# Optimization experiments

Hardware: AMD Instinct MI355X
Metric: run time of the kernel (lower is better)

## Reference

```python
import jax, jax.numpy as jnp
import numpy as np

B, CIN, H, W = 2, 192, 56, 56
ODIM, HEADS, K, PAD, STRIDE = 192, 6, 7, 3, 1


def setup_inputs() -> dict:
    key = jax.random.key(0)
    ks = jax.random.split(key, 6)
    w_scale = 0.02
    return {
        "x": jax.random.normal(ks[0], (B, CIN, H, W), dtype=jnp.float32),
        "wq": jax.random.normal(ks[1], (ODIM, CIN), dtype=jnp.float32) * w_scale,
        "wk": jax.random.normal(ks[2], (ODIM, CIN), dtype=jnp.float32) * w_scale,
        "wv": jax.random.normal(ks[3], (ODIM, CIN), dtype=jnp.float32) * w_scale,
        "pos_embedding": jax.random.normal(ks[4], (1, 2 * K - 1), dtype=jnp.float32),
        "w_proj": jax.random.normal(ks[5], (ODIM, ODIM), dtype=jnp.float32) * w_scale,
        "kernel_size": K,
        "padding": PAD,
        "stride": STRIDE,
        "num_heads": HEADS,
    }


def _patches(x, k, pad, stride):
    # torch.nn.Unfold(kernel_size=k, padding=pad, stride=stride), kept as
    # (B, C, k*k, oh, ow) with window offsets ordered row-major (i*k + j),
    # channel slowest -- matching torch's (C, kh, kw) flattening.
    xp = jnp.pad(x, ((0, 0), (0, 0), (pad, pad), (pad, pad)))
    Hp, Wp = xp.shape[2], xp.shape[3]
    oh = (Hp - k) // stride + 1
    ow = (Wp - k) // stride + 1
    sl = [xp[:, :, i:i + stride * (oh - 1) + 1:stride, j:j + stride * (ow - 1) + 1:stride]
          for i in range(k) for j in range(k)]
    return jnp.stack(sl, axis=2)


def reference(x, wq, wk, wv, pos_embedding, w_proj, kernel_size, padding, stride, num_heads):
    b, c, h, w = x.shape
    # 1x1 convs (no bias) == channel matmuls
    q = jnp.einsum('oc,bchw->bohw', wq, x)
    k = jnp.einsum('oc,bchw->bohw', wk, x)
    v = jnp.einsum('oc,bchw->bohw', wv, x)
    # Unfold(kernel=1, stride=s) on q == strided spatial subsampling
    q = q[:, :, ::stride, ::stride]
    kp = _patches(k, kernel_size, padding, stride)  # (B, O, K*K, oh, ow)
    vp = _patches(v, kernel_size, padding, stride)
    oh, ow = kp.shape[3], kp.shape[4]
    d = wq.shape[0] // num_heads
    kk = kernel_size * kernel_size
    qh = q.reshape(b, num_heads, d, oh, ow)
    kh = kp.reshape(b, num_heads, d, kk, oh, ow)
    vh = vp.reshape(b, num_heads, d, kk, oh, ow)
    # per-pixel windowed attention scores: (B, heads, K*K, oh, ow)
    attn = jnp.einsum('bhdij,bhdkij->bhkij', qh, kh)
    # relative position bias: index = row_offset + col_offset (0 .. 2K-2)
    coords = np.arange(kernel_size)
    rel = (coords[:, None] + coords[None, :]).reshape(-1)  # (K*K,)
    bias = pos_embedding[0][jnp.asarray(rel)]  # (K*K,)
    attn = jax.nn.softmax(attn + bias[None, None, :, None, None], axis=2)
    out = jnp.einsum('bhkij,bhdkij->bhdij', attn, vh)
    out = out.reshape(b, num_heads * d, oh, ow)
    return jnp.einsum('oc,bchw->bohw', w_proj, out)
```

## Files before the change

### kernel.cpp

```cpp
#include <hip/hip_runtime.h>


#define HW    3136
#define WIMG  56
#define CIN   192
#define QKVLD 576

using short8 = __attribute__((ext_vector_type(8))) short;
using f32x4  = __attribute__((ext_vector_type(4))) float;

__device__ __forceinline__ unsigned short f2bf(float f) {
    union { float f; unsigned int u; } v; v.f = f;
    unsigned int r = v.u + 0x7fffu + ((v.u >> 16) & 1u);
    return (unsigned short)(r >> 16);
}

__global__ __launch_bounds__(256) void prep_kernel(
    const float* __restrict__ x,  const float* __restrict__ wq,
    const float* __restrict__ wk, const float* __restrict__ wv,
    const float* __restrict__ wproj,
    unsigned short* __restrict__ xt, unsigned short* __restrict__ wb)
{
    const int tid = threadIdx.x;
    if (blockIdx.z == 2) {
        int gid  = blockIdx.y * 49 + blockIdx.x;
        int base = (gid * 256 + tid) * 4;
        if (base < 147456) {
            const float* src;
            if      (base <  36864) src = wq    + base;
            else if (base <  73728) src = wk    + base -  36864;
            else if (base < 110592) src = wv    + base -  73728;
            else                    src = wproj + base - 110592;
            float4 v = *(const float4*)src;
            ushort4 h;
            h.x = f2bf(v.x); h.y = f2bf(v.y); h.z = f2bf(v.z); h.w = f2bf(v.w);
            *(ushort4*)(wb + base) = h;
        }
        return;
    }
    __shared__ float t[64][68];
    const int b  = blockIdx.z;
    const int p0 = blockIdx.x * 64, c0 = blockIdx.y * 64;
    {
        const int r0 = tid >> 4, pq = (tid & 15) * 4;
        #pragma unroll
        for (int i = 0; i < 4; ++i) {
            int cc = r0 + 16 * i;
            float4 v = *(const float4*)(x + (size_t)(b * CIN + c0 + cc) * HW + p0 + pq);
            *(float4*)&t[cc][pq] = v;
        }
    }
    __syncthreads();
    #pragma unroll
    for (int i = 0; i < 2; ++i) {
        int u = tid + 256 * i;
        int pr = u >> 3, oct = u & 7;
        ushort4 h0, h1;
        h0.x = f2bf(t[oct*8+0][pr]); h0.y = f2bf(t[oct*8+1][pr]);
        h0.z = f2bf(t[oct*8+2][pr]); h0.w = f2bf(t[oct*8+3][pr]);
        h1.x = f2bf(t[oct*8+4][pr]); h1.y = f2bf(t[oct*8+5][pr]);
        h1.z = f2bf(t[oct*8+6][pr]); h1.w = f2bf(t[oct*8+7][pr]);
        unsigned short* dst = xt + ((size_t)(b * HW + p0 + pr) * CIN + c0 + oct * 8);
        *(ushort4*)dst       = h0;
        *(ushort4*)(dst + 4) = h1;
    }
}

__global__ __launch_bounds__(256) void gemm64(
    const unsigned short* __restrict__ A, long Ab,
    const unsigned short* __restrict__ B, long Bb,
    float* __restrict__ Y, long Yb, int ldY)
{
    __shared__ unsigned short As[64 * 200];
    __shared__ unsigned short Bs[64 * 200];
    const int tid = threadIdx.x;

    A += blockIdx.z * Ab + (size_t)blockIdx.x * 64 * CIN;
    B += blockIdx.z * Bb + (size_t)blockIdx.y * 64 * CIN;
    Y += blockIdx.z * Yb + (size_t)blockIdx.x * 64 * ldY + blockIdx.y * 64;

    const int r = tid >> 2, c4 = tid & 3;
    #pragma unroll
    for (int i = 0; i < 6; ++i) {
        int oct = c4 + 4 * i;
        *(uint4*)(As + r * 200 + oct * 8) = *(const uint4*)(A + r * CIN + oct * 8);
        *(uint4*)(Bs + r * 200 + oct * 8) = *(const uint4*)(B + r * CIN + oct * 8);
    }
    __syncthreads();

    const int lane = tid & 63, wave = tid >> 6;
    const int wm = (wave & 1) * 32, wn = (wave >> 1) * 32;
    const int l15 = lane & 15, quad = lane >> 4;

    f32x4 acc[2][2] = {};
    const unsigned short* pa0 = As + (wm + l15) * 200 + quad * 8;
    const unsigned short* pb0 = Bs + (wn + l15) * 200 + quad * 8;

    #pragma unroll
    for (int s = 0; s < 6; ++s) {
        short8 a0 = *(const short8*)(pa0 + s * 32);
        short8 a1 = *(const short8*)(pa0 + 16 * 200 + s * 32);
        short8 b0 = *(const short8*)(pb0 + s * 32);
        short8 b1 = *(const short8*)(pb0 + 16 * 200 + s * 32);
        acc[0][0] = __builtin_amdgcn_mfma_f32_16x16x32_bf16(a0, b0, acc[0][0], 0, 0, 0);
        acc[0][1] = __builtin_amdgcn_mfma_f32_16x16x32_bf16(a0, b1, acc[0][1], 0, 0, 0);
        acc[1][0] = __builtin_amdgcn_mfma_f32_16x16x32_bf16(a1, b0, acc[1][0], 0, 0, 0);
        acc[1][1] = __builtin_amdgcn_mfma_f32_16x16x32_bf16(a1, b1, acc[1][1], 0, 0, 0);
    }

    #pragma unroll
    for (int ti = 0; ti < 2; ++ti)
        #pragma unroll
        for (int tj = 0; tj < 2; ++tj)
            #pragma unroll
            for (int rr = 0; rr < 4; ++rr) {
                int row = wm + ti * 16 + quad * 4 + rr;
                int col = wn + tj * 16 + l15;
                Y[(size_t)row * ldY + col] = acc[ti][tj][rr];
            }
}

__global__ __launch_bounds__(256) void attn_kernel(
    const float* __restrict__ qkv, const float* __restrict__ pos,
    unsigned short* __restrict__ oact)
{
    __shared__ float kbuf[196 * 34];
    __shared__ float vbuf[196 * 34];

    const int tid = threadIdx.x;
    const int tx = blockIdx.x, ty = blockIdx.y;
    const int b = blockIdx.z / 6, h = blockIdx.z % 6;
    const int y0 = ty * 8 - 3, x0 = tx * 8 - 3;
    const int chk = 192 + h * 32, chv = 384 + h * 32;

    for (int ii = tid; ii < 3136; ii += 256) {
        int pp = ii >> 4, u = ii & 15;
        int py = pp / 14, px = pp - py * 14;
        int gy = y0 + py, gx = x0 + px;
        int isv = u >> 3, uu = u & 7;
        float4 val = make_float4(0.f, 0.f, 0.f, 0.f);
        if ((unsigned)gy < 56u && (unsigned)gx < 56u) {
            int p = gy * WIMG + gx;
            val = *(const float4*)(qkv + (size_t)(b * HW + p) * QKVLD + (isv ? chv : chk) + uu * 4);
        }
        float* dst = (isv ? vbuf : kbuf) + pp * 34 + uu * 4;
        *(float2*)dst       = make_float2(val.x, val.y);
        *(float2*)(dst + 2) = make_float2(val.z, val.w);
    }
    __syncthreads();

    const int sub = tid & 3, pix = tid >> 2;
    const int py = pix >> 3, px = pix & 7;
    const int y = ty * 8 + py, x = tx * 8 + px;
    const int p = y * WIMG + x;

    const float* qb = qkv + (size_t)(b * HW + p) * QKVLD + h * 32 + sub * 8;
    float4 q0 = *(const float4*)qb, q1 = *(const float4*)(qb + 4);

    float posr[13];
    #pragma unroll
    for (int i = 0; i < 13; ++i) posr[i] = pos[i];

    float logits[49];
    #pragma unroll
    for (int kk = 0; kk < 49; ++kk) {
        const int ky = kk / 7, kx = kk % 7;
        const int pp = (py + ky) * 14 + (px + kx);
        const float2* kp = (const float2*)(kbuf + pp * 34 + sub * 8);
        float2 k0 = kp[0], k1 = kp[1], k2 = kp[2], k3 = kp[3];
        float s = 0.f;
        s = fmaf(q0.x, k0.x, s); s = fmaf(q0.y, k0.y, s);
        s = fmaf(q0.z, k1.x, s); s = fmaf(q0.w, k1.y, s);
        s = fmaf(q1.x, k2.x, s); s = fmaf(q1.y, k2.y, s);
        s = fmaf(q1.z, k3.x, s); s = fmaf(q1.w, k3.y, s);
        s += __shfl_xor(s, 1);
        s += __shfl_xor(s, 2);
        logits[kk] = s + posr[ky + kx];
    }

    float m = logits[0];
    #pragma unroll
    for (int kk = 1; kk < 49; ++kk) m = fmaxf(m, logits[kk]);
    float sum = 0.f;
    #pragma unroll
    for (int kk = 0; kk < 49; ++kk) {
        logits[kk] = __expf(logits[kk] - m);
        sum += logits[kk];
    }
    const float inv = 1.f / sum;

    float acc[8] = {};
    #pragma unroll
    for (int kk = 0; kk < 49; ++kk) {
        const int ky = kk / 7, kx = kk % 7;
        const int pp = (py + ky) * 14 + (px + kx);
        const float2* vp = (const float2*)(vbuf + pp * 34 + sub * 8);
        float2 v0 = vp[0], v1 = vp[1], v2 = vp[2], v3 = vp[3];
        const float pw = logits[kk] * inv;
        acc[0] = fmaf(pw, v0.x, acc[0]); acc[1] = fmaf(pw, v0.y, acc[1]);
        acc[2] = fmaf(pw, v1.x, acc[2]); acc[3] = fmaf(pw, v1.y, acc[3]);
        acc[4] = fmaf(pw, v2.x, acc[4]); acc[5] = fmaf(pw, v2.y, acc[5]);
        acc[6] = fmaf(pw, v3.x, acc[6]); acc[7] = fmaf(pw, v3.y, acc[7]);
    }

    ushort4 h0, h1;
    h0.x = f2bf(acc[0]); h0.y = f2bf(acc[1]); h0.z = f2bf(acc[2]); h0.w = f2bf(acc[3]);
    h1.x = f2bf(acc[4]); h1.y = f2bf(acc[5]); h1.z = f2bf(acc[6]); h1.w = f2bf(acc[7]);
    unsigned short* ob = oact + ((size_t)(b * HW + p) * CIN + h * 32 + sub * 8);
    *(ushort4*)ob       = h0;
    *(ushort4*)(ob + 4) = h1;
}

extern "C" void kernel_launch(void* const* d_in, const int* in_sizes, int n_in,
                              void* d_out, int out_size, void* d_ws, size_t ws_size,
                              hipStream_t stream)
{
    const float* x     = (const float*)d_in[0];
    const float* wq    = (const float*)d_in[1];
    const float* wk    = (const float*)d_in[2];
    const float* wv    = (const float*)d_in[3];
    const float* pos   = (const float*)d_in[4];
    const float* wproj = (const float*)d_in[5];

    char* ws = (char*)d_ws;
    unsigned short* xt   = (unsigned short*)(ws);
    unsigned short* wb   = (unsigned short*)(ws + 2408448);
    float*          qkv  = (float*)        (ws + 2703360);
    unsigned short* oact = (unsigned short*)(ws + 17154048);
    float* out = (float*)d_out;

    prep_kernel<<<dim3(49, 3, 3), 256, 0, stream>>>(x, wq, wk, wv, wproj, xt, wb);
    gemm64<<<dim3(49, 9, 2), 256, 0, stream>>>(
        xt, (long)HW * CIN, wb, 0L, qkv, (long)HW * QKVLD, QKVLD);
    attn_kernel<<<dim3(7, 7, 12), 256, 0, stream>>>(qkv, pos, oact);
    gemm64<<<dim3(3, 49, 2), 256, 0, stream>>>(
        wb + 576 * CIN, 0L, oact, (long)HW * CIN, out, (long)CIN * HW, HW);
}
```

Before: 113.4 us.

## Fuse pipeline into one cooperative persistent kernel with grid syncs and bf16 QK

Replaces the four launches (prep, QKV GEMM, attention, projection GEMM) with one cooperative persistent kernel of 256 blocks that loops over tiles in three phases separated by grid.sync. The fp32-to-bf16 conversion of x and the weights now happens inside the GEMM tile loads, so the separate prep pass and its workspace traffic go away. Q and K are stored as bf16 while V stays fp32, which halves the Q/K intermediate traffic at some cost in precision. The aim is to cut launch overhead and memory round trips, at the price of grid-wide barriers and only 256 resident blocks doing all the work. A plain multi-kernel fallback runs if the cooperative launch fails.

```diff
diff --git a/kernel.cpp b/kernel.cpp
--- a/kernel.cpp
+++ b/kernel.cpp
@@ -1,101 +1,82 @@
 #include <hip/hip_runtime.h>
+#include <hip/hip_cooperative_groups.h>
+
+namespace cg = cooperative_groups;
 
 
 #define HW    3136
 #define WIMG  56
 #define CIN   192
-#define QKVLD 576
+#define QKLD  384
+#define SMEM_BYTES 53312
 
 using short8 = __attribute__((ext_vector_type(8))) short;
 using f32x4  = __attribute__((ext_vector_type(4))) float;
 
 __device__ __forceinline__ unsigned short f2bf(float f) {
-    union { float f; unsigned int u; } v; v.f = f;
-    unsigned int r = v.u + 0x7fffu + ((v.u >> 16) & 1u);
+    union { float f; unsigned u; } v; v.f = f;
+    unsigned r = v.u + 0x7fffu + ((v.u >> 16) & 1u);
     return (unsigned short)(r >> 16);
 }
-
-__global__ __launch_bounds__(256) void prep_kernel(
-    const float* __restrict__ x,  const float* __restrict__ wq,
+__device__ __forceinline__ unsigned pack2(float a, float b) {
+    return (unsigned)f2bf(a) | ((unsigned)f2bf(b) << 16);
+}
+__device__ __forceinline__ float bflo(unsigned u) {
+    union { unsigned u; float f; } v; v.u = u << 16; return v.f;
+}
+__device__ __forceinline__ float bfhi(unsigned u) {
+    union { unsigned u; float f; } v; v.u = u & 0xffff0000u; return v.f;
+}
+
+__device__ __forceinline__ void phase1_qkv(
+    int t, int tid, const float* __restrict__ x, const float* __restrict__ wq,
     const float* __restrict__ wk, const float* __restrict__ wv,
-    const float* __restrict__ wproj,
-    unsigned short* __restrict__ xt, unsigned short* __restrict__ wb)
-{
-    const int tid = threadIdx.x;
-    if (blockIdx.z == 2) {
-        int gid  = blockIdx.y * 49 + blockIdx.x;
-        int base = (gid * 256 + tid) * 4;
-        if (base < 147456) {
-            const float* src;
-            if      (base <  36864) src = wq    + base;
-            else if (base <  73728) src = wk    + base -  36864;
-            else if (base < 110592) src = wv    + base -  73728;
-            else                    src = wproj + base - 110592;
-            float4 v = *(const float4*)src;
-            ushort4 h;
-            h.x = f2bf(v.x); h.y = f2bf(v.y); h.z = f2bf(v.z); h.w = f2bf(v.w);
-            *(ushort4*)(wb + base) = h;
-        }
-        return;
-    }
-    __shared__ float t[64][68];
-    const int b  = blockIdx.z;
-    const int p0 = blockIdx.x * 64, c0 = blockIdx.y * 64;
+    unsigned short* __restrict__ qk, float* __restrict__ vv, char* smem)
+{
+    unsigned short* As  = (unsigned short*)smem;
+    unsigned short* Bs  = As + 64 * 200;
+    unsigned*       Asw = (unsigned*)smem;
+    unsigned*       Bsw = (unsigned*)(smem + 25600);
+
+    const int lane = tid & 63, wave = tid >> 6;
+    const int l15  = lane & 15, quad = lane >> 4;
+    const int wm   = (wave & 1) * 32, wn = (wave >> 1) * 32;
+
+    const int mt = t % 98, nt = t / 98;
+    const int m0 = mt * 64, n0 = nt * 64;
+    const float* Wp = (nt < 3) ? (wq + (size_t)n0 * CIN)
+                    : (nt < 6) ? (wk + (size_t)(n0 - 192) * CIN)
+                               : (wv + (size_t)(n0 - 384) * CIN);
+
+    #pragma unroll
+    for (int i = 0; i < 6; ++i) {
+        int u = tid + 256 * i;
+        int pq = u & 15, c2 = u >> 4;
+        int pp = m0 + pq * 4;
+        int bb = (pp >= HW) ? 1 : 0;
+        const float* src = x + ((size_t)(bb * CIN + c2 * 2)) * HW + (pp - bb * HW);
+        float4 f0 = *(const float4*)src;
+        float4 f1 = *(const float4*)(src + HW);
+        Asw[(pq * 4 + 0) * 100 + c2] = pack2(f0.x, f1.x);
+        Asw[(pq * 4 + 1) * 100 + c2] = pack2(f0.y, f1.y);
+        Asw[(pq * 4 + 2) * 100 + c2] = pack2(f0.z, f1.z);
+        Asw[(pq * 4 + 3) * 100 + c2] = pack2(f0.w, f1.w);
+    }
     {
-        const int r0 = tid >> 4, pq = (tid & 15) * 4;
-        #pragma unroll
-        for (int i = 0; i < 4; ++i) {
-            int cc = r0 + 16 * i;
-            float4 v = *(const float4*)(x + (size_t)(b * CIN + c0 + cc) * HW + p0 + pq);
-            *(float4*)&t[cc][pq] = v;
+        int o = tid >> 2, c4 = tid & 3;
+        #pragma unroll
+        for (int i = 0; i < 12; ++i) {
+            int cq = c4 + 4 * i;
+            float4 w = *(const float4*)(Wp + (size_t)o * CIN + cq * 4);
+            uint2 d; d.x = pack2(w.x, w.y); d.y = pack2(w.z, w.w);
+            *(uint2*)(Bsw + o * 100 + cq * 2) = d;
         }
     }
     __syncthreads();
-    #pragma unroll
-    for (int i = 0; i < 2; ++i) {
-        int u = tid + 256 * i;
-        int pr = u >> 3, oct = u & 7;
-        ushort4 h0, h1;
-        h0.x = f2bf(t[oct*8+0][pr]); h0.y = f2bf(t[oct*8+1][pr]);
-        h0.z = f2bf(t[oct*8+2][pr]); h0.w = f2bf(t[oct*8+3][pr]);
-        h1.x = f2bf(t[oct*8+4][pr]); h1.y = f2bf(t[oct*8+5][pr]);
-        h1.z = f2bf(t[oct*8+6][pr]); h1.w = f2bf(t[oct*8+7][pr]);
-        unsigned short* dst = xt + ((size_t)(b * HW + p0 + pr) * CIN + c0 + oct * 8);
-        *(ushort4*)dst       = h0;
-        *(ushort4*)(dst + 4) = h1;
-    }
-}
-
-__global__ __launch_bounds__(256) void gemm64(
-    const unsigned short* __restrict__ A, long Ab,
-    const unsigned short* __restrict__ B, long Bb,
-    float* __restrict__ Y, long Yb, int ldY)
-{
-    __shared__ unsigned short As[64 * 200];
-    __shared__ unsigned short Bs[64 * 200];
-    const int tid = threadIdx.x;
-
-    A += blockIdx.z * Ab + (size_t)blockIdx.x * 64 * CIN;
-    B += blockIdx.z * Bb + (size_t)blockIdx.y * 64 * CIN;
-    Y += blockIdx.z * Yb + (size_t)blockIdx.x * 64 * ldY + blockIdx.y * 64;
-
-    const int r = tid >> 2, c4 = tid & 3;
-    #pragma unroll
-    for (int i = 0; i < 6; ++i) {
-        int oct = c4 + 4 * i;
-        *(uint4*)(As + r * 200 + oct * 8) = *(const uint4*)(A + r * CIN + oct * 8);
-        *(uint4*)(Bs + r * 200 + oct * 8) = *(const uint4*)(B + r * CIN + oct * 8);
-    }
-    __syncthreads();
-
-    const int lane = tid & 63, wave = tid >> 6;
-    const int wm = (wave & 1) * 32, wn = (wave >> 1) * 32;
-    const int l15 = lane & 15, quad = lane >> 4;
 
     f32x4 acc[2][2] = {};
     const unsigned short* pa0 = As + (wm + l15) * 200 + quad * 8;
     const unsigned short* pb0 = Bs + (wn + l15) * 200 + quad * 8;
-
     #pragma unroll
     for (int s = 0; s < 6; ++s) {
         short8 a0 = *(const short8*)(pa0 + s * 32);
@@ -108,54 +89,89 @@
         acc[1][1] = __builtin_amdgcn_mfma_f32_16x16x32_bf16(a1, b1, acc[1][1], 0, 0, 0);
     }
 
-    #pragma unroll
-    for (int ti = 0; ti < 2; ++ti)
-        #pragma unroll
-        for (int tj = 0; tj < 2; ++tj)
+    const int gm = m0 + wm + quad * 4;
+    const int gn = n0 + wn + l15;
+    if (nt < 6) {
+        #pragma unroll
+        for (int ti = 0; ti < 2; ++ti)
             #pragma unroll
-            for (int rr = 0; rr < 4; ++rr) {
-                int row = wm + ti * 16 + quad * 4 + rr;
-                int col = wn + tj * 16 + l15;
-                Y[(size_t)row * ldY + col] = acc[ti][tj][rr];
+            for (int tj = 0; tj < 2; ++tj)
+                #pragma unroll
+                for (int rr = 0; rr < 4; ++rr)
+                    qk[(size_t)(gm + ti * 16 + rr) * QKLD + (gn + tj * 16)] =
+                        f2bf(acc[ti][tj][rr]);
+    } else {
+        #pragma unroll
+        for (int ti = 0; ti < 2; ++ti)
+            #pragma unroll
+            for (int tj = 0; tj < 2; ++tj)
+                #pragma unroll
+                for (int rr = 0; rr < 4; ++rr)
+                    vv[(size_t)(gm + ti * 16 + rr) * CIN + (gn + tj * 16 - 384)] =
+                        acc[ti][tj][rr];
+    }
+}
+
+__device__ __forceinline__ void phase2_attn(
+    int t, int tid, const unsigned short* __restrict__ qk,
+    const float* __restrict__ vv, const float* __restrict__ pos,
+    unsigned short* __restrict__ oact, char* smem)
+{
+    float* kbuf = (float*)smem;
+    float* vbuf = kbuf + 6664;
+
+    const int tz = t / 49, r49 = t - tz * 49;
+    const int ty = r49 / 7, tx = r49 - ty * 7;
+    const int bq = tz / 6, h = tz - bq * 6;
+    const int y0 = ty * 8 - 3, x0 = tx * 8 - 3;
+
+    #pragma unroll
+    for (int i = 0; i < 4; ++i) {
+        int u = tid + 256 * i;
+        if (u < 784) {
+            int pp = u >> 2, uu = u & 3;
+            int py = pp / 14, px = pp - py * 14;
+            int gy = y0 + py, gx = x0 + px;
+            float f0=0,f1=0,f2=0,f3=0,f4=0,f5=0,f6=0,f7=0;
+            if ((unsigned)gy < 56u && (unsigned)gx < 56u) {
+                uint4 rv = *(const uint4*)(qk +
+                    (size_t)(bq * HW + gy * WIMG + gx) * QKLD + 192 + h * 32 + uu * 8);
+                f0=bflo(rv.x); f1=bfhi(rv.x); f2=bflo(rv.y); f3=bfhi(rv.y);
+                f4=bflo(rv.z); f5=bfhi(rv.z); f6=bflo(rv.w); f7=bfhi(rv.w);
             }
-}
-
-__global__ __launch_bounds__(256) void attn_kernel(
-    const float* __restrict__ qkv, const float* __restrict__ pos,
-    unsigned short* __restrict__ oact)
-{
-    __shared__ float kbuf[196 * 34];
-    __shared__ float vbuf[196 * 34];
-
-    const int tid = threadIdx.x;
-    const int tx = blockIdx.x, ty = blockIdx.y;
-    const int b = blockIdx.z / 6, h = blockIdx.z % 6;
-    const int y0 = ty * 8 - 3, x0 = tx * 8 - 3;
-    const int chk = 192 + h * 32, chv = 384 + h * 32;
-
-    for (int ii = tid; ii < 3136; ii += 256) {
-        int pp = ii >> 4, u = ii & 15;
-        int py = pp / 14, px = pp - py * 14;
-        int gy = y0 + py, gx = x0 + px;
-        int isv = u >> 3, uu = u & 7;
-        float4 val = make_float4(0.f, 0.f, 0.f, 0.f);
-        if ((unsigned)gy < 56u && (unsigned)gx < 56u) {
-            int p = gy * WIMG + gx;
-            val = *(const float4*)(qkv + (size_t)(b * HW + p) * QKVLD + (isv ? chv : chk) + uu * 4);
-        }
-        float* dst = (isv ? vbuf : kbuf) + pp * 34 + uu * 4;
-        *(float2*)dst       = make_float2(val.x, val.y);
-        *(float2*)(dst + 2) = make_float2(val.z, val.w);
+            float* dst = kbuf + pp * 34 + uu * 8;
+            *(float2*)(dst + 0) = make_float2(f0, f1);
+            *(float2*)(dst + 2) = make_float2(f2, f3);
+            *(float2*)(dst + 4) = make_float2(f4, f5);
+            *(float2*)(dst + 6) = make_float2(f6, f7);
+        }
+    }
+    #pragma unroll
+    for (int i = 0; i < 7; ++i) {
+        int u = tid + 256 * i;
+        if (u < 1568) {
+            int pp = u >> 3, uu = u & 7;
+            int py = pp / 14, px = pp - py * 14;
+            int gy = y0 + py, gx = x0 + px;
+            float4 val = make_float4(0.f, 0.f, 0.f, 0.f);
+            if ((unsigned)gy < 56u && (unsigned)gx < 56u)
+                val = *(const float4*)(vv +
+                    (size_t)(bq * HW + gy * WIMG + gx) * CIN + h * 32 + uu * 4);
+            float* dst = vbuf + pp * 34 + uu * 4;
+            *(float2*)(dst + 0) = make_float2(val.x, val.y);
+            *(float2*)(dst + 2) = make_float2(val.z, val.w);
+        }
     }
     __syncthreads();
 
     const int sub = tid & 3, pix = tid >> 2;
     const int py = pix >> 3, px = pix & 7;
-    const int y = ty * 8 + py, x = tx * 8 + px;
-    const int p = y * WIMG + x;
-
-    const float* qb = qkv + (size_t)(b * HW + p) * QKVLD + h * 32 + sub * 8;
-    float4 q0 = *(const float4*)qb, q1 = *(const float4*)(qb + 4);
+    const int y = ty * 8 + py, xx = tx * 8 + px;
+    const int p = y * WIMG + xx;
+
+    uint4 qv = *(const uint4*)(qk + (size_t)(bq * HW + p) * QKLD + h * 32 + sub * 8);
+    float q0=bflo(qv.x), q1=bfhi(qv.x), q2=bflo(qv.y), q3=bfhi(qv.y);
+    float q4=bflo(qv.z), q5=bfhi(qv.z), q6=bflo(qv.w), q7=bfhi(qv.w);
 
     float posr[13];
     #pragma unroll
@@ -169,10 +185,10 @@
         const float2* kp = (const float2*)(kbuf + pp * 34 + sub * 8);
         float2 k0 = kp[0], k1 = kp[1], k2 = kp[2], k3 = kp[3];
         float s = 0.f;
-        s = fmaf(q0.x, k0.x, s); s = fmaf(q0.y, k0.y, s);
-        s = fmaf(q0.z, k1.x, s); s = fmaf(q0.w, k1.y, s);
-        s = fmaf(q1.x, k2.x, s); s = fmaf(q1.y, k2.y, s);
-        s = fmaf(q1.z, k3.x, s); s = fmaf(q1.w, k3.y, s);
+        s = fmaf(q0, k0.x, s); s = fmaf(q1, k0.y, s);
+        s = fmaf(q2, k1.x, s); s = fmaf(q3, k1.y, s);
+        s = fmaf(q4, k2.x, s); s = fmaf(q5, k2.y, s);
+        s = fmaf(q6, k3.x, s); s = fmaf(q7, k3.y, s);
         s += __shfl_xor(s, 1);
         s += __shfl_xor(s, 2);
         logits[kk] = s + posr[ky + kx];
@@ -189,7 +205,7 @@
     }
     const float inv = 1.f / sum;
 
-    float acc[8] = {};
+    float a0=0,a1=0,a2=0,a3=0,a4=0,a5=0,a6=0,a7=0;
     #pragma unroll
     for (int kk = 0; kk < 49; ++kk) {
         const int ky = kk / 7, kx = kk % 7;
@@ -197,18 +213,132 @@
         const float2* vp = (const float2*)(vbuf + pp * 34 + sub * 8);
         float2 v0 = vp[0], v1 = vp[1], v2 = vp[2], v3 = vp[3];
         const float pw = logits[kk] * inv;
-        acc[0] = fmaf(pw, v0.x, acc[0]); acc[1] = fmaf(pw, v0.y, acc[1]);
-        acc[2] = fmaf(pw, v1.x, acc[2]); acc[3] = fmaf(pw, v1.y, acc[3]);
-        acc[4] = fmaf(pw, v2.x, acc[4]); acc[5] = fmaf(pw, v2.y, acc[5]);
-        acc[6] = fmaf(pw, v3.x, acc[6]); acc[7] = fmaf(pw, v3.y, acc[7]);
+        a0 = fmaf(pw, v0.x, a0); a1 = fmaf(pw, v0.y, a1);
+        a2 = fmaf(pw, v1.x, a2); a3 = fmaf(pw, v1.y, a3);
+        a4 = fmaf(pw, v2.x, a4); a5 = fmaf(pw, v2.y, a5);
+        a6 = fmaf(pw, v3.x, a6); a7 = fmaf(pw, v3.y, a7);
     }
 
     ushort4 h0, h1;
-    h0.x = f2bf(acc[0]); h0.y = f2bf(acc[1]); h0.z = f2bf(acc[2]); h0.w = f2bf(acc[3]);
-    h1.x = f2bf(acc[4]); h1.y = f2bf(acc[5]); h1.z = f2bf(acc[6]); h1.w = f2bf(acc[7]);
-    unsigned short* ob = oact + ((size_t)(b * HW + p) * CIN + h * 32 + sub * 8);
+    h0.x = f2bf(a0); h0.y = f2bf(a1); h0.z = f2bf(a2); h0.w = f2bf(a3);
+    h1.x = f2bf(a4); h1.y = f2bf(a5); h1.z = f2bf(a6); h1.w = f2bf(a7);
+    unsigned short* ob = oact + (size_t)(bq * HW + p) * CIN + h * 32 + sub * 8;
     *(ushort4*)ob       = h0;
     *(ushort4*)(ob + 4) = h1;
+}
+
+__device__ __forceinline__ void phase3_proj(
+    int t, int tid, const float* __restrict__ wproj,
+    const unsigned short* __restrict__ oact, float* __restrict__ out, char* smem)
+{
+    unsigned short* As  = (unsigned short*)smem;
+    unsigned short* Bs  = As + 64 * 200;
+    unsigned*       Asw = (unsigned*)smem;
+
+    const int lane = tid & 63, wave = tid >> 6;
+    const int l15  = lane & 15, quad = lane >> 4;
+    const int wm   = (wave & 1) * 32, wn = (wave >> 1) * 32;
+
+    const int mt = t % 3, pt = t / 3;
+    {
+        int o = tid >> 2, c4 = tid & 3;
+        #pragma unroll
+        for (int i = 0; i < 12; ++i) {
+            int cq = c4 + 4 * i;
+            float4 w = *(const float4*)(wproj + (size_t)(mt * 64 + o) * CIN + cq * 4);
+            uint2 d; d.x = pack2(w.x, w.y); d.y = pack2(w.z, w.w);
+            *(uint2*)(Asw + o * 100 + cq * 2) = d;
+        }
+    }
+    {
+        int rw = tid >> 2, s4 = tid & 3;
+        #pragma unroll
+        for (int i = 0; i < 6; ++i) {
+            int seg = s4 + 4 * i;
+            uint4 dv = *(const uint4*)(oact + (size_t)(pt * 64 + rw) * CIN + seg * 8);
+            *(uint4*)(Bs + rw * 200 + seg * 8) = dv;
+        }
+    }
+    __syncthreads();
+
+    f32x4 acc[2][2] = {};
+    const unsigned short* pa0 = As + (wm + l15) * 200 + quad * 8;
+    const unsigned short* pb0 = Bs + (wn + l15) * 200 + quad * 8;
+    #pragma unroll
+    for (int s = 0; s < 6; ++s) {
+        short8 a0 = *(const short8*)(pa0 + s * 32);
+        short8 a1 = *(const short8*)(pa0 + 16 * 200 + s * 32);
+        short8 b0 = *(const short8*)(pb0 + s * 32);
+        short8 b1 = *(const short8*)(pb0 + 16 * 200 + s * 32);
+        acc[0][0] = __builtin_amdgcn_mfma_f32_16x16x32_bf16(a0, b0, acc[0][0], 0, 0, 0);
+        acc[0][1] = __builtin_amdgcn_mfma_f32_16x16x32_bf16(a0, b1, acc[0][1], 0, 0, 0);
+        acc[1][0] = __builtin_amdgcn_mfma_f32_16x16x32_bf16(a1, b0, acc[1][0], 0, 0, 0);
+        acc[1][1] = __builtin_amdgcn_mfma_f32_16x16x32_bf16(a1, b1, acc[1][1], 0, 0, 0);
+    }
+
+    const int bb = (pt * 64 >= HW) ? 1 : 0;
+    const int pl = pt * 64 - bb * HW + wn + l15;
+    const int go = mt * 64 + wm + quad * 4;
+    float* Yb = out + (size_t)bb * (CIN * HW);
+    #pragma unroll
+    for (int ti = 0; ti < 2; ++ti)
+        #pragma unroll
+        for (int tj = 0; tj < 2; ++tj)
+            #pragma unroll
+            for (int rr = 0; rr < 4; ++rr)
+                Yb[(size_t)(go + ti * 16 + rr) * HW + pl + tj * 16] = acc[ti][tj][rr];
+}
+
+__global__ __launch_bounds__(256) void fused_sasa(
+    const float* __restrict__ x, const float* __restrict__ wq,
+    const float* __restrict__ wk, const float* __restrict__ wv,
+    const float* __restrict__ wproj, const float* __restrict__ pos,
+    unsigned short* __restrict__ qk, float* __restrict__ vv,
+    unsigned short* __restrict__ oact, float* __restrict__ out)
+{
+    extern __shared__ char smem[];
+    cg::grid_group grid = cg::this_grid();
+    const int tid = threadIdx.x, nb = gridDim.x;
+
+    for (int t = blockIdx.x; t < 882; t += nb) {
+        phase1_qkv(t, tid, x, wq, wk, wv, qk, vv, smem);
+        __syncthreads();
+    }
+    grid.sync();
+    for (int t = blockIdx.x; t < 588; t += nb) {
+        phase2_attn(t, tid, qk, vv, pos, oact, smem);
+        __syncthreads();
+    }
+    grid.sync();
+    for (int t = blockIdx.x; t < 294; t += nb) {
+        phase3_proj(t, tid, wproj, oact, out, smem);
+        __syncthreads();
+    }
+}
+
+__global__ __launch_bounds__(256) void k_p1(
+    const float* __restrict__ x, const float* __restrict__ wq,
+    const float* __restrict__ wk, const float* __restrict__ wv,
+    unsigned short* __restrict__ qk, float* __restrict__ vv)
+{
+    extern __shared__ char smem[];
+    phase1_qkv(blockIdx.x, threadIdx.x, x, wq, wk, wv, qk, vv, smem);
+}
+
+__global__ __launch_bounds__(256) void k_p2(
+    const unsigned short* __restrict__ qk, const float* __restrict__ vv,
+    const float* __restrict__ pos, unsigned short* __restrict__ oact)
+{
+    extern __shared__ char smem[];
+    phase2_attn(blockIdx.x, threadIdx.x, qk, vv, pos, oact, smem);
+}
+
+__global__ __launch_bounds__(256) void k_p3(
+    const float* __restrict__ wproj, const unsigned short* __restrict__ oact,
+    float* __restrict__ out)
+{
+    extern __shared__ char smem[];
+    phase3_proj(blockIdx.x, threadIdx.x, wproj, oact, out, smem);
 }
 
 extern "C" void kernel_launch(void* const* d_in, const int* in_sizes, int n_in,
@@ -223,16 +353,19 @@
     const float* wproj = (const float*)d_in[5];
 
     char* ws = (char*)d_ws;
-    unsigned short* xt   = (unsigned short*)(ws);
-    unsigned short* wb   = (unsigned short*)(ws + 2408448);
-    float*          qkv  = (float*)        (ws + 2703360);
-    unsigned short* oact = (unsigned short*)(ws + 17154048);
-    float* out = (float*)d_out;
-
-    prep_kernel<<<dim3(49, 3, 3), 256, 0, stream>>>(x, wq, wk, wv, wproj, xt, wb);
-    gemm64<<<dim3(49, 9, 2), 256, 0, stream>>>(
-        xt, (long)HW * CIN, wb, 0L, qkv, (long)HW * QKVLD, QKVLD);
-    attn_kernel<<<dim3(7, 7, 12), 256, 0, stream>>>(qkv, pos, oact);
-    gemm64<<<dim3(3, 49, 2), 256, 0, stream>>>(
-        wb + 576 * CIN, 0L, oact, (long)HW * CIN, out, (long)CIN * HW, HW);
-}
+    unsigned short* qkp   = (unsigned short*)ws;
+    float*          vvp   = (float*)(ws + 4816896);
+    unsigned short* oactp = (unsigned short*)(ws + 9633792);
+    float*          outp  = (float*)d_out;
+
+    void* args[10] = { (void*)&x, (void*)&wq, (void*)&wk, (void*)&wv, (void*)&wproj,
+                       (void*)&pos, (void*)&qkp, (void*)&vvp, (void*)&oactp, (void*)&outp };
+    hipError_t rc = hipLaunchCooperativeKernel(fused_sasa, dim3(256), dim3(256),
+                                               args, (unsigned)SMEM_BYTES, stream);
+    if (rc != hipSuccess) {
+        (void)hipGetLastError();
+        k_p1<<<dim3(882), dim3(256), SMEM_BYTES, stream>>>(x, wq, wk, wv, qkp, vvp);
+        k_p2<<<dim3(588), dim3(256), SMEM_BYTES, stream>>>(qkp, vvp, pos, oactp);
+        k_p3<<<dim3(294), dim3(256), SMEM_BYTES, stream>>>(wproj, oactp, outp);
+    }
+}
```

After: 199.1 us. +75.6%, slower.
